# Kernel tuning notes

Hardware: AMD Instinct MI355X
Metric: run time of the kernel (lower is better)

Reference implementation:

```python
import jax, jax.numpy as jnp
import numpy as np

N, D, C = 4096, 512, 64
MARGIN = 1.0
INF = jnp.float32(1e30)


def setup_inputs() -> dict:
    key = jax.random.key(0)
    k1, k2 = jax.random.split(key)
    embeddings = jax.random.normal(k1, (N, D), dtype=jnp.float32)
    targets = jax.random.randint(k2, (N,), 0, C)
    return {"embeddings": embeddings, "targets": targets}


def _triplet_loss(embeddings, targets, margin=MARGIN):
    # Squared pairwise distances [N, N] (differentiable, used for the loss)
    sq_norms = jnp.sum(embeddings * embeddings, axis=1)
    sq_dist = jnp.maximum(
        sq_norms[:, None] + sq_norms[None, :] - 2.0 * (embeddings @ embeddings.T), 0.0
    )
    # Euclidean distances for mining only (index selection is non-differentiable in torch)
    dist = jnp.sqrt(jax.lax.stop_gradient(sq_dist))

    same = targets[:, None] == targets[None, :]  # [N, N] same-label mask

    # Hardest negative per anchor: argmax_k (d_ap - d_ak + margin) == argmin_k d_ak over negatives
    neg_dist = jnp.where(same, INF, dist)
    n_idx = jnp.argmin(neg_dist, axis=1)   # [N] hardest negative index per anchor
    min_neg = jnp.min(neg_dist, axis=1)    # [N] its euclidean distance

    idx = jnp.arange(dist.shape[0])
    # anchor-positive pairs: same label, a < p (torch.combinations on sorted indices)
    pair_mask = same & (idx[:, None] < idx[None, :])
    # triplet kept only if mined loss (euclidean) strictly positive
    valid = pair_mask & (dist - min_neg[:, None] + margin > 0)

    ap_sq = sq_dist                         # [N, N] squared anchor-positive distances
    an_sq = sq_dist[idx, n_idx]             # [N]   squared anchor-hard-negative distances
    losses = jax.nn.relu(ap_sq - an_sq[:, None] + margin)

    cnt = jnp.sum(valid)
    denom = jnp.maximum(cnt, 1).astype(losses.dtype)
    loss = jnp.sum(jnp.where(valid, losses, 0.0)) / denom

    correct = jnp.sum(valid & (ap_sq < an_sq[:, None]))
    accuracy = correct.astype(jnp.float32) / jnp.maximum(cnt, 1).astype(jnp.float32)
    return loss, accuracy


def reference(embeddings, targets):
    return _triplet_loss(embeddings, targets)
```

## Files before the change

kernel.cpp:

```cpp
#include <hip/hip_runtime.h>

#define N 4096
#define D 512
#define C 64
#define MARGIN 1.0f
#define TILE 128
#define ROWB 128
#define NTILES (N / TILE)
#define NTRI (NTILES * (NTILES + 1) / 2)
#define FINF 3.0e38f
#define SLOTW 16
#define PCAP 1024
#define LOSSB 128

typedef __attribute__((ext_vector_type(8))) short short8;
typedef __attribute__((ext_vector_type(4))) float floatx4;

__device__ __forceinline__ unsigned short f2bf(float f) {
  unsigned int u = __float_as_uint(f);
  u += 0x7FFFu + ((u >> 16) & 1u);
  return (unsigned short)(u >> 16);
}

__device__ __forceinline__ void gload_lds16(const void* g, void* l) {
  __builtin_amdgcn_global_load_lds(
      (const __attribute__((address_space(1))) unsigned int*)g,
      (__attribute__((address_space(3))) unsigned int*)l, 16, 0, 0);
}

__global__ __launch_bounds__(256) void prep_kernel(const float* __restrict__ E,
                                                   unsigned short* __restrict__ Ebf,
                                                   float* __restrict__ norms,
                                                   unsigned int* __restrict__ an_sq_bits,
                                                   unsigned int* __restrict__ accs_u,
                                                   unsigned int* __restrict__ ctrl) {
  const int row = blockIdx.x;
  const int tid = threadIdx.x;
  if (row == N) {
    for (int k = tid; k < C * SLOTW; k += 256) accs_u[k] = 0u;
    if (tid < 2) ctrl[tid] = 0u;
    return;
  }
  if (row < 16) an_sq_bits[row * 256 + tid] = 0x7F800000u;
  const float2 v = reinterpret_cast<const float2*>(E + (size_t)row * D)[tid];
  float s = v.x * v.x + v.y * v.y;
  unsigned int packed = ((unsigned int)f2bf(v.y) << 16) | (unsigned int)f2bf(v.x);
  reinterpret_cast<unsigned int*>(Ebf + (size_t)row * D)[tid] = packed;
  for (int off = 32; off > 0; off >>= 1) s += __shfl_down(s, off);
  __shared__ float wsum[4];
  if ((tid & 63) == 0) wsum[tid >> 6] = s;
  __syncthreads();
  if (tid == 0) norms[row] = wsum[0] + wsum[1] + wsum[2] + wsum[3];
}

__global__ __launch_bounds__(256, 3) void gemm_min_kernel(const unsigned short* __restrict__ Ebf,
                                                          const float* __restrict__ norms,
                                                          const int* __restrict__ targets,
                                                          unsigned int* __restrict__ an_sq_bits,
                                                          uint2* __restrict__ pairs,
                                                          unsigned int* __restrict__ ctrl) {
  const int u = blockIdx.x;
  int i = (int)((sqrtf(8.0f * (float)u + 1.0f) - 1.0f) * 0.5f);
  while ((i + 1) * (i + 2) / 2 <= u) ++i;
  while (i * (i + 1) / 2 > u) --i;
  const int tm = u - i * (i + 1) / 2;
  const int tn = i;

  __shared__ alignas(16) unsigned char As[TILE * ROWB];
  __shared__ alignas(16) unsigned char Bs[TILE * ROWB];
  __shared__ float s_rmin[2][TILE];
  __shared__ float s_cmin[2][TILE];
  __shared__ unsigned int s_pkey[PCAP];
  __shared__ float s_psq[PCAP];
  __shared__ unsigned int s_pcnt, s_pbase;

  const int tid = threadIdx.x;
  const int wave = tid >> 6, lane = tid & 63;
  const int quad = lane >> 4, l16 = lane & 15;
  const int wr = wave >> 1, wc = wave & 1;
  const int rowBase = tm * TILE, colBase = tn * TILE;
  if (tid == 0) s_pcnt = 0u;

  const int lr = lane >> 3;
  const int lq = (lane & 7) ^ lr;
  const int lofs = lr * (D * 2) + lq * 16;
  const unsigned char* gA = (const unsigned char*)Ebf + (size_t)rowBase * (D * 2);
  const unsigned char* gB = (const unsigned char*)Ebf + (size_t)colBase * (D * 2);

  const int swz = l16 & 7;
  int rA[4], rB[4], cq[2];
#pragma unroll
  for (int s = 0; s < 4; s++) {
    rA[s] = (wr * 64 + s * 16 + l16) * ROWB;
    rB[s] = (wc * 64 + s * 16 + l16) * ROWB;
  }
#pragma unroll
  for (int ks = 0; ks < 2; ks++) cq[ks] = ((ks * 4 + quad) ^ swz) * 16;

  floatx4 acc[4][4];
#pragma unroll
  for (int a = 0; a < 4; a++)
#pragma unroll
    for (int b = 0; b < 4; b++) acc[a][b] = (floatx4){0.f, 0.f, 0.f, 0.f};

  for (int k0b = 0; k0b < D * 2; k0b += 128) {
#pragma unroll
    for (int t = 0; t < 4; t++) {
      const int g = wave * 4 + t;
      gload_lds16(gA + (size_t)g * 8 * (D * 2) + lofs + k0b, As + g * 1024);
      gload_lds16(gB + (size_t)g * 8 * (D * 2) + lofs + k0b, Bs + g * 1024);
    }
    __syncthreads();
#pragma unroll
    for (int ks = 0; ks < 2; ks++) {
      short8 af[4], bf[4];
#pragma unroll
      for (int s = 0; s < 4; s++) {
        af[s] = *reinterpret_cast<const short8*>(As + rA[s] + cq[ks]);
        bf[s] = *reinterpret_cast<const short8*>(Bs + rB[s] + cq[ks]);
      }
#pragma unroll
      for (int sm = 0; sm < 4; sm++)
#pragma unroll
        for (int sn = 0; sn < 4; sn++)
          acc[sm][sn] = __builtin_amdgcn_mfma_f32_16x16x32_bf16(af[sm], bf[sn], acc[sm][sn], 0, 0, 0);
    }
    __syncthreads();
  }

  int tcol[4], gcolv[4];
  float ncol[4];
#pragma unroll
  for (int sn = 0; sn < 4; sn++) {
    const int gc = colBase + wc * 64 + sn * 16 + l16;
    gcolv[sn] = gc;
    tcol[sn] = targets[gc];
    ncol[sn] = norms[gc];
  }
  float colmin[4] = {FINF, FINF, FINF, FINF};
#pragma unroll
  for (int sm = 0; sm < 4; sm++) {
#pragma unroll
    for (int r = 0; r < 4; r++) {
      const int rloc = wr * 64 + sm * 16 + quad * 4 + r;
      const int grow = rowBase + rloc;
      const int trow = targets[grow];
      const float nrow = norms[grow];
      float rowmin = FINF;
#pragma unroll
      for (int sn = 0; sn < 4; sn++) {
        const float sq = fmaxf(nrow + ncol[sn] - 2.0f * acc[sm][sn][r], 0.0f);
        if (tcol[sn] != trow) {
          rowmin = fminf(rowmin, sq);
          colmin[sn] = fminf(colmin[sn], sq);
        } else if (grow < gcolv[sn]) {
          const unsigned int idx = atomicAdd(&s_pcnt, 1u);
          if (idx < PCAP) {
            s_pkey[idx] = ((unsigned int)grow << 12) | (unsigned int)gcolv[sn];
            s_psq[idx] = sq;
          } else {
            const unsigned int g = atomicAdd(&ctrl[0], 1u);
            pairs[g] = make_uint2(((unsigned int)grow << 12) | (unsigned int)gcolv[sn],
                                  __float_as_uint(sq));
          }
        }
      }
#pragma unroll
      for (int off = 1; off < 16; off <<= 1) rowmin = fminf(rowmin, __shfl_xor(rowmin, off));
      if (l16 == 0) s_rmin[wc][rloc] = rowmin;
    }
  }
#pragma unroll
  for (int sn = 0; sn < 4; sn++) {
    float cm = colmin[sn];
    cm = fminf(cm, __shfl_xor(cm, 16));
    cm = fminf(cm, __shfl_xor(cm, 32));
    if (quad == 0) s_cmin[wr][wc * 64 + sn * 16 + l16] = cm;
  }
  __syncthreads();
  if (tid < TILE) {
    const float m = fminf(s_rmin[0][tid], s_rmin[1][tid]);
    if (m < FINF) atomicMin(&an_sq_bits[rowBase + tid], __float_as_uint(m));
  } else {
    const int c = tid - TILE;
    const float m = fminf(s_cmin[0][c], s_cmin[1][c]);
    if (m < FINF) atomicMin(&an_sq_bits[colBase + c], __float_as_uint(m));
  }
  const unsigned int npair = min(s_pcnt, (unsigned int)PCAP);
  if (tid == 0) s_pbase = atomicAdd(&ctrl[0], npair);
  __syncthreads();
  for (unsigned int r = tid; r < npair; r += 256)
    pairs[s_pbase + r] = make_uint2(s_pkey[r], __float_as_uint(s_psq[r]));
}

__global__ __launch_bounds__(256) void loss_kernel(const uint2* __restrict__ pairs,
                                                   const unsigned int* __restrict__ an_sq_bits,
                                                   float* __restrict__ accs,
                                                   unsigned int* __restrict__ ctrl,
                                                   float* __restrict__ out) {
  const int tid = threadIdx.x, wave = tid >> 6, lane = tid & 63;
  const unsigned int M = ctrl[0];
  __shared__ float s_sum[4];
  __shared__ unsigned int s_cnt[4], s_cor[4];
  __shared__ int s_last;
  float bsum = 0.f;
  unsigned int bcnt = 0, bcor = 0;
  for (unsigned int r = blockIdx.x * 256 + tid; r < M; r += LOSSB * 256) {
    const uint2 rec = pairs[r];
    const int a = (int)(rec.x >> 12);
    const float sq = __uint_as_float(rec.y);
    const float an = __uint_as_float(an_sq_bits[a]);
    if (sqrtf(sq) - sqrtf(an) + MARGIN > 0.0f) {
      bcnt++;
      bsum += fmaxf(sq - an + MARGIN, 0.0f);
      if (sq < an) bcor++;
    }
  }
#pragma unroll
  for (int off = 32; off > 0; off >>= 1) {
    bsum += __shfl_down(bsum, off);
    bcnt += __shfl_down(bcnt, off);
    bcor += __shfl_down(bcor, off);
  }
  if (lane == 0) { s_sum[wave] = bsum; s_cnt[wave] = bcnt; s_cor[wave] = bcor; }
  __syncthreads();
  if (tid == 0) {
    float* slot = accs + (size_t)(blockIdx.x & (C - 1)) * SLOTW;
    atomicAdd(&slot[0], s_sum[0] + s_sum[1] + s_sum[2] + s_sum[3]);
    atomicAdd((unsigned int*)&slot[1], s_cnt[0] + s_cnt[1] + s_cnt[2] + s_cnt[3]);
    atomicAdd((unsigned int*)&slot[2], s_cor[0] + s_cor[1] + s_cor[2] + s_cor[3]);
    __threadfence();
    s_last = (atomicAdd(&ctrl[1], 1u) == (unsigned int)LOSSB - 1u);
  }
  __syncthreads();
  if (s_last) {
    __threadfence();
    if (tid < C) {
      float sum = __uint_as_float(atomicAdd((unsigned int*)&accs[(size_t)tid * SLOTW + 0], 0u));
      unsigned int cnt = atomicAdd((unsigned int*)&accs[(size_t)tid * SLOTW + 1], 0u);
      unsigned int cor = atomicAdd((unsigned int*)&accs[(size_t)tid * SLOTW + 2], 0u);
#pragma unroll
      for (int off = 32; off > 0; off >>= 1) {
        sum += __shfl_down(sum, off);
        cnt += __shfl_down(cnt, off);
        cor += __shfl_down(cor, off);
      }
      if (tid == 0) {
        const float denom = (float)(cnt > 0u ? cnt : 1u);
        out[0] = sum / denom;
        out[1] = (float)cor / denom;
      }
    }
  }
}

extern "C" void kernel_launch(void* const* d_in, const int* in_sizes, int n_in,
                              void* d_out, int out_size, void* d_ws, size_t ws_size,
                              hipStream_t stream) {
  const float* E = (const float*)d_in[0];
  const int* targets = (const int*)d_in[1];
  float* out = (float*)d_out;
  char* ws = (char*)d_ws;
  size_t off = 0;
  unsigned short* Ebf = (unsigned short*)(ws + off); off += (size_t)N * D * 2;
  float* norms = (float*)(ws + off); off += (size_t)N * 4;
  unsigned int* an_sq = (unsigned int*)(ws + off); off += (size_t)N * 4;
  float* accs = (float*)(ws + off); off += (size_t)C * SLOTW * 4;
  unsigned int* ctrl = (unsigned int*)(ws + off); off += 256;
  uint2* pairs = (uint2*)(ws + off);

  prep_kernel<<<dim3(N + 1), dim3(256), 0, stream>>>(E, Ebf, norms, an_sq, (unsigned int*)accs, ctrl);
  gemm_min_kernel<<<dim3(NTRI), dim3(256), 0, stream>>>(Ebf, norms, targets, an_sq, pairs, ctrl);
  loss_kernel<<<dim3(LOSSB), dim3(256), 0, stream>>>(pairs, an_sq, accs, ctrl, out);
}
```

Baseline: 95.24 us.

## Load GEMM fragments directly from global memory, dropping LDS staging

Result: slower. 125.8 us (+32.1%).

```diff
diff --git a/kernel.cpp b/kernel.cpp
--- a/kernel.cpp
+++ b/kernel.cpp
@@ -5,7 +5,6 @@
 #define C 64
 #define MARGIN 1.0f
 #define TILE 128
-#define ROWB 128
 #define NTILES (N / TILE)
 #define NTRI (NTILES * (NTILES + 1) / 2)
 #define FINF 3.0e38f
@@ -20,12 +19,6 @@
   unsigned int u = __float_as_uint(f);
   u += 0x7FFFu + ((u >> 16) & 1u);
   return (unsigned short)(u >> 16);
-}
-
-__device__ __forceinline__ void gload_lds16(const void* g, void* l) {
-  __builtin_amdgcn_global_load_lds(
-      (const __attribute__((address_space(1))) unsigned int*)g,
-      (__attribute__((address_space(3))) unsigned int*)l, 16, 0, 0);
 }
 
 __global__ __launch_bounds__(256) void prep_kernel(const float* __restrict__ E,
@@ -53,7 +46,7 @@
   if (tid == 0) norms[row] = wsum[0] + wsum[1] + wsum[2] + wsum[3];
 }
 
-__global__ __launch_bounds__(256, 3) void gemm_min_kernel(const unsigned short* __restrict__ Ebf,
+__global__ __launch_bounds__(256, 2) void gemm_min_kernel(const unsigned short* __restrict__ Ebf,
                                                           const float* __restrict__ norms,
                                                           const int* __restrict__ targets,
                                                           unsigned int* __restrict__ an_sq_bits,
@@ -66,8 +59,6 @@
   const int tm = u - i * (i + 1) / 2;
   const int tn = i;
 
-  __shared__ alignas(16) unsigned char As[TILE * ROWB];
-  __shared__ alignas(16) unsigned char Bs[TILE * ROWB];
   __shared__ float s_rmin[2][TILE];
   __shared__ float s_cmin[2][TILE];
   __shared__ unsigned int s_pkey[PCAP];
@@ -81,21 +72,15 @@
   const int rowBase = tm * TILE, colBase = tn * TILE;
   if (tid == 0) s_pcnt = 0u;
 
-  const int lr = lane >> 3;
-  const int lq = (lane & 7) ^ lr;
-  const int lofs = lr * (D * 2) + lq * 16;
-  const unsigned char* gA = (const unsigned char*)Ebf + (size_t)rowBase * (D * 2);
-  const unsigned char* gB = (const unsigned char*)Ebf + (size_t)colBase * (D * 2);
-
-  const int swz = l16 & 7;
-  int rA[4], rB[4], cq[2];
+  const unsigned char* pA[4];
+  const unsigned char* pB[4];
 #pragma unroll
   for (int s = 0; s < 4; s++) {
-    rA[s] = (wr * 64 + s * 16 + l16) * ROWB;
-    rB[s] = (wc * 64 + s * 16 + l16) * ROWB;
-  }
-#pragma unroll
-  for (int ks = 0; ks < 2; ks++) cq[ks] = ((ks * 4 + quad) ^ swz) * 16;
+    pA[s] = (const unsigned char*)Ebf +
+            (size_t)(rowBase + wr * 64 + s * 16 + l16) * (D * 2) + quad * 16;
+    pB[s] = (const unsigned char*)Ebf +
+            (size_t)(colBase + wc * 64 + s * 16 + l16) * (D * 2) + quad * 16;
+  }
 
   floatx4 acc[4][4];
 #pragma unroll
@@ -103,21 +88,16 @@
 #pragma unroll
     for (int b = 0; b < 4; b++) acc[a][b] = (floatx4){0.f, 0.f, 0.f, 0.f};
 
-  for (int k0b = 0; k0b < D * 2; k0b += 128) {
-#pragma unroll
-    for (int t = 0; t < 4; t++) {
-      const int g = wave * 4 + t;
-      gload_lds16(gA + (size_t)g * 8 * (D * 2) + lofs + k0b, As + g * 1024);
-      gload_lds16(gB + (size_t)g * 8 * (D * 2) + lofs + k0b, Bs + g * 1024);
-    }
-    __syncthreads();
+#pragma unroll
+  for (int c = 0; c < 8; ++c) {
 #pragma unroll
     for (int ks = 0; ks < 2; ks++) {
+      const int off = c * 128 + ks * 64;
       short8 af[4], bf[4];
 #pragma unroll
       for (int s = 0; s < 4; s++) {
-        af[s] = *reinterpret_cast<const short8*>(As + rA[s] + cq[ks]);
-        bf[s] = *reinterpret_cast<const short8*>(Bs + rB[s] + cq[ks]);
+        af[s] = *reinterpret_cast<const short8*>(pA[s] + off);
+        bf[s] = *reinterpret_cast<const short8*>(pB[s] + off);
       }
 #pragma unroll
       for (int sm = 0; sm < 4; sm++)
@@ -125,7 +105,6 @@
         for (int sn = 0; sn < 4; sn++)
           acc[sm][sn] = __builtin_amdgcn_mfma_f32_16x16x32_bf16(af[sm], bf[sn], acc[sm][sn], 0, 0, 0);
     }
-    __syncthreads();
   }
 
   int tcol[4], gcolv[4];
```
